# Kernel tuning notes

Hardware: AMD Instinct MI355X
Metric: run time of the kernel (lower is better)

## Reference

```python
import jax, jax.numpy as jnp
import numpy as np

G = 4      # num_groups
I = 128    # per-group input dim  (input_dim // num_groups)
H = 128    # per-group hidden dim (hidden_dim // num_groups)
B, T = 32, 1000


def setup_inputs() -> dict:
    key = jax.random.key(0)
    k0, k1, k2, k3, k4 = jax.random.split(key, 5)
    s = 1.0 / np.sqrt(H)  # PyTorch GRU init scale
    x = jax.random.normal(k0, (B, T, G * I), dtype=jnp.float32)
    w_ih = jax.random.uniform(k1, (G, 3 * H, I), jnp.float32, -s, s)
    w_hh = jax.random.uniform(k2, (G, 3 * H, H), jnp.float32, -s, s)
    b_ih = jax.random.uniform(k3, (G, 3 * H), jnp.float32, -s, s)
    b_hh = jax.random.uniform(k4, (G, 3 * H), jnp.float32, -s, s)
    return {"x": x, "w_ih": w_ih, "w_hh": w_hh, "b_ih": b_ih, "b_hh": b_hh}


def reference(x, w_ih, w_hh, b_ih, b_hh):
    # x: [B, T, G*I]. Chunking along dim 2 == reshape to [B, T, G, I].
    Bx, Tx, _ = x.shape
    xg = x.reshape(Bx, Tx, G, I)
    # Precompute input projections for all timesteps/groups (block-diagonal GEMM).
    gi = jnp.einsum('btgi,gki->btgk', xg, w_ih) + b_ih  # [B, T, G, 3H]

    def step(h, gi_t):
        # h: [B, G, H]; gi_t: [B, G, 3H]
        gh = jnp.einsum('bgh,gkh->bgk', h, w_hh) + b_hh  # [B, G, 3H]
        i_r, i_z, i_n = jnp.split(gi_t, 3, axis=-1)
        h_r, h_z, h_n = jnp.split(gh, 3, axis=-1)
        r = jax.nn.sigmoid(i_r + h_r)
        z = jax.nn.sigmoid(i_z + h_z)
        n = jnp.tanh(i_n + r * h_n)
        h_new = (1.0 - z) * n + z * h
        return h_new, h_new

    h0 = jnp.zeros((Bx, G, H), dtype=x.dtype)
    _, ys = jax.lax.scan(step, h0, jnp.swapaxes(gi, 0, 1))  # [T, B, G, H]
    # Concat of group outputs along dim 2 == reshape [B, T, G*H].
    return jnp.swapaxes(ys, 0, 1).reshape(Bx, Tx, G * H)
```

## Files before the change

### kernel.cpp

```cpp
#include <hip/hip_runtime.h>
#include <hip/hip_bf16.h>

#define NG 4
#define ID 128
#define HD 128
#define TH 384
#define NB 32
#define NT 1000
#define XW (NG*ID)
#define OW (NG*HD)

typedef _Float16 v8h __attribute__((ext_vector_type(8)));
typedef __attribute__((ext_vector_type(4))) float v4f;

__device__ __forceinline__ float sigm(float v) {
    return __fdividef(1.f, 1.f + __expf(-v));
}
__device__ __forceinline__ float tanh_(float v) {
    v = fminf(fmaxf(v, -15.f), 15.f);
    float e2 = __expf(2.f * v);
    return __fdividef(e2 - 1.f, e2 + 1.f);
}
__device__ __forceinline__ float sel4(v4f a, int s) {
    float x01 = (s & 1) ? a[1] : a[0];
    float x23 = (s & 1) ? a[3] : a[2];
    return (s & 2) ? x23 : x01;
}
__device__ __forceinline__ void gl2lds16(const void* g, void* l) {
    __builtin_amdgcn_global_load_lds(
        (const __attribute__((address_space(1))) unsigned int*)g,
        (__attribute__((address_space(3))) unsigned int*)l, 16, 0, 0);
}

__global__ __launch_bounds__(256) void gi_gemm4(
    const float* __restrict__ x,
    const float* __restrict__ w_ih,
    const float* __restrict__ b_ih,
    _Float16* __restrict__ gi_ws)
{
    const int tid = threadIdx.x;
    const int w   = tid >> 6, l = tid & 63;
    const int lr  = l & 15, lq = l >> 4;
    const int g   = blockIdx.z;
    const int b   = blockIdx.y >> 3;
    const int tt  = blockIdx.y & 7;
    const int gate = blockIdx.x;
    const int n0  = gate * 128 + (w >> 1) * 64;
    const int t0  = tt * 128 + (w & 1) * 64;

    v4f acc[4][4];
    #pragma unroll
    for (int mi = 0; mi < 4; ++mi)
        #pragma unroll
        for (int ni = 0; ni < 4; ++ni)
            acc[mi][ni] = (v4f){0.f, 0.f, 0.f, 0.f};

    #pragma unroll
    for (int kf = 0; kf < 4; ++kf) {
        v8h bf[4], af[4];
        #pragma unroll
        for (int ni = 0; ni < 4; ++ni) {
            const float* p = &w_ih[(size_t)(g * TH + n0 + ni * 16 + lr) * ID + kf * 32 + lq * 8];
            float4 f0 = *reinterpret_cast<const float4*>(p);
            float4 f1 = *reinterpret_cast<const float4*>(p + 4);
            v8h v;
            v[0]=(_Float16)f0.x; v[1]=(_Float16)f0.y; v[2]=(_Float16)f0.z; v[3]=(_Float16)f0.w;
            v[4]=(_Float16)f1.x; v[5]=(_Float16)f1.y; v[6]=(_Float16)f1.z; v[7]=(_Float16)f1.w;
            bf[ni] = v;
        }
        #pragma unroll
        for (int mi = 0; mi < 4; ++mi) {
            int trow = t0 + mi * 16 + lr;
            int tl = trow < NT ? trow : NT - 1;
            const float* p = &x[((size_t)b * NT + tl) * XW + g * ID + kf * 32 + lq * 8];
            float4 f0 = *reinterpret_cast<const float4*>(p);
            float4 f1 = *reinterpret_cast<const float4*>(p + 4);
            v8h v;
            v[0]=(_Float16)f0.x; v[1]=(_Float16)f0.y; v[2]=(_Float16)f0.z; v[3]=(_Float16)f0.w;
            v[4]=(_Float16)f1.x; v[5]=(_Float16)f1.y; v[6]=(_Float16)f1.z; v[7]=(_Float16)f1.w;
            af[mi] = v;
        }
        #pragma unroll
        for (int mi = 0; mi < 4; ++mi)
            #pragma unroll
            for (int ni = 0; ni < 4; ++ni)
                acc[mi][ni] = __builtin_amdgcn_mfma_f32_16x16x32_f16(
                    af[mi], bf[ni], acc[mi][ni], 0, 0, 0);
    }

    const size_t rbase = (size_t)(b * NG + g) * NT;
    #pragma unroll
    for (int ni = 0; ni < 4; ++ni) {
        const int col = n0 + ni * 16 + lr;
        const float bias = b_ih[g * TH + col];
        const int jj = col & 127;
        const int off = (gate == 0) ? jj * 2 : (gate == 1) ? jj * 2 + 1 : 256 + jj;
        #pragma unroll
        for (int mi = 0; mi < 4; ++mi) {
            #pragma unroll
            for (int r = 0; r < 4; ++r) {
                const int t = t0 + mi * 16 + lq * 4 + r;
                if (t < NT)
                    gi_ws[(rbase + t) * 384 + off] = (_Float16)(acc[mi][ni][r] + bias);
            }
        }
    }
}

__global__ __launch_bounds__(512) void gru_rec8(
    const _Float16* __restrict__ gi_ws,
    const float* __restrict__ w_hh,
    const float* __restrict__ b_hh,
    float* __restrict__ out)
{
    __shared__ __align__(16) _Float16 h_lds[2][128];
    __shared__ __align__(16) _Float16 tile[2][3072];

    const int tid = threadIdx.x;
    const int w = tid >> 6, l = tid & 63;
    const int lr = l & 15, lq = l >> 4;
    const int g = blockIdx.x & 3;
    const int b = blockIdx.x >> 2;

    v8h a[3][4];
    #pragma unroll
    for (int i = 0; i < 3; ++i) {
        const int mrow = i * 128 + 16 * w + lr;
        #pragma unroll
        for (int kf = 0; kf < 4; ++kf) {
            const float* p = &w_hh[(size_t)(g * TH + mrow) * HD + kf * 32 + lq * 8];
            float4 f0 = *reinterpret_cast<const float4*>(p);
            float4 f1 = *reinterpret_cast<const float4*>(p + 4);
            v8h v;
            v[0]=(_Float16)f0.x; v[1]=(_Float16)f0.y; v[2]=(_Float16)f0.z; v[3]=(_Float16)f0.w;
            v[4]=(_Float16)f1.x; v[5]=(_Float16)f1.y; v[6]=(_Float16)f1.z; v[7]=(_Float16)f1.w;
            a[i][kf] = v;
        }
    }

    const int sel = l & 3;
    const int j   = 16 * w + 4 * lq + sel;
    const bool active = ((l >> 2) & 3) == 0;
    const v4f bv0 = *reinterpret_cast<const v4f*>(&b_hh[g * TH +       16 * w + 4 * lq]);
    const v4f bv1 = *reinterpret_cast<const v4f*>(&b_hh[g * TH + 128 + 16 * w + 4 * lq]);
    const v4f bv2 = *reinterpret_cast<const v4f*>(&b_hh[g * TH + 256 + 16 * w + 4 * lq]);
    float hprev = 0.f;
    float* outp = out + (size_t)b * NT * OW + g * HD + j;

    if (tid < 128) { h_lds[0][tid] = (_Float16)0.f; h_lds[1][tid] = (_Float16)0.f; }

    const _Float16* gsrc = gi_ws + (size_t)(b * NG + g) * NT * 384;
    if (tid < 384) gl2lds16(gsrc + tid * 8, &tile[0][tid * 8]);
    __syncthreads();

    float hv[8];
    for (int T = 0; T < 125; ++T) {
        const int cbuf = T & 1;
        if (T < 124 && tid < 384)
            gl2lds16(gsrc + (size_t)(T + 1) * 3072 + tid * 8, &tile[cbuf ^ 1][tid * 8]);
        #pragma unroll
        for (int k = 0; k < 8; ++k) {
            const char* hb = reinterpret_cast<const char*>(&h_lds[k & 1][0]) + lq * 16;
            v8h f0 = *reinterpret_cast<const v8h*>(hb);
            v8h f1 = *reinterpret_cast<const v8h*>(hb + 64);
            v8h f2 = *reinterpret_cast<const v8h*>(hb + 128);
            v8h f3 = *reinterpret_cast<const v8h*>(hb + 192);
            v4f ac0 = bv0, ac1 = bv1, ac2 = bv2;
            ac0 = __builtin_amdgcn_mfma_f32_16x16x32_f16(a[0][0], f0, ac0, 0, 0, 0);
            ac1 = __builtin_amdgcn_mfma_f32_16x16x32_f16(a[1][0], f0, ac1, 0, 0, 0);
            ac2 = __builtin_amdgcn_mfma_f32_16x16x32_f16(a[2][0], f0, ac2, 0, 0, 0);
            ac0 = __builtin_amdgcn_mfma_f32_16x16x32_f16(a[0][1], f1, ac0, 0, 0, 0);
            ac1 = __builtin_amdgcn_mfma_f32_16x16x32_f16(a[1][1], f1, ac1, 0, 0, 0);
            ac2 = __builtin_amdgcn_mfma_f32_16x16x32_f16(a[2][1], f1, ac2, 0, 0, 0);
            ac0 = __builtin_amdgcn_mfma_f32_16x16x32_f16(a[0][2], f2, ac0, 0, 0, 0);
            ac1 = __builtin_amdgcn_mfma_f32_16x16x32_f16(a[1][2], f2, ac1, 0, 0, 0);
            ac2 = __builtin_amdgcn_mfma_f32_16x16x32_f16(a[2][2], f2, ac2, 0, 0, 0);
            ac0 = __builtin_amdgcn_mfma_f32_16x16x32_f16(a[0][3], f3, ac0, 0, 0, 0);
            ac1 = __builtin_amdgcn_mfma_f32_16x16x32_f16(a[1][3], f3, ac1, 0, 0, 0);
            ac2 = __builtin_amdgcn_mfma_f32_16x16x32_f16(a[2][3], f3, ac2, 0, 0, 0);

            float ghr = sel4(ac0, sel);
            float ghz = sel4(ac1, sel);
            float ghn = sel4(ac2, sel);

            const char* gl = reinterpret_cast<const char*>(&tile[cbuf][k * 384]);
            unsigned int rz = *reinterpret_cast<const unsigned int*>(gl + j * 4);
            float iN = (float)*reinterpret_cast<const _Float16*>(gl + 512 + j * 2);
            float iR = (float)__builtin_bit_cast(_Float16, (unsigned short)(rz & 0xffff));
            float iZ = (float)__builtin_bit_cast(_Float16, (unsigned short)(rz >> 16));

            float rr = sigm(iR + ghr);
            float zz = sigm(iZ + ghz);
            float nn = tanh_(fmaf(rr, ghn, iN));
            float hn = fmaf(zz, hprev - nn, nn);
            hprev = hn;
            hv[k] = hn;
            if (active) h_lds[(k + 1) & 1][j] = (_Float16)hn;
            __syncthreads();
        }
        if (active) {
            const size_t ob = (size_t)(T * 8) * OW;
            #pragma unroll
            for (int k = 0; k < 8; ++k)
                outp[ob + (size_t)k * OW] = hv[k];
        }
    }
}

extern "C" void kernel_launch(void* const* d_in, const int* in_sizes, int n_in,
                              void* d_out, int out_size, void* d_ws, size_t ws_size,
                              hipStream_t stream) {
    const float* x    = (const float*)d_in[0];
    const float* w_ih = (const float*)d_in[1];
    const float* w_hh = (const float*)d_in[2];
    const float* b_ih = (const float*)d_in[3];
    const float* b_hh = (const float*)d_in[4];
    float* out = (float*)d_out;
    _Float16* gi_ws = (_Float16*)d_ws;

    dim3 g1(3, NB * 8, NG);
    gi_gemm4<<<g1, 256, 0, stream>>>(x, w_ih, b_ih, gi_ws);
    gru_rec8<<<NB * NG, 512, 0, stream>>>(gi_ws, w_hh, b_hh, out);
}
```

Measured before the change: 581.4 us.

## Prefetch input gates into registers and replace syncthreads with LDS-only barrier

Removes the LDS double-buffered tile of precomputed input gates and instead has each thread load its own r/z/n values from global memory two timesteps ahead into registers. The per-step __syncthreads is replaced by an explicit lgkmcnt(0) wait plus s_barrier, so the barrier does not wait on outstanding global loads or stores. Output stores are issued per step rather than batched every 8 steps. This aims to shorten the serial per-step critical path, at the risk of global-load latency exceeding the two-step prefetch distance.

```diff
diff --git a/kernel.cpp b/kernel.cpp
--- a/kernel.cpp
+++ b/kernel.cpp
@@ -25,11 +25,6 @@
     float x01 = (s & 1) ? a[1] : a[0];
     float x23 = (s & 1) ? a[3] : a[2];
     return (s & 2) ? x23 : x01;
-}
-__device__ __forceinline__ void gl2lds16(const void* g, void* l) {
-    __builtin_amdgcn_global_load_lds(
-        (const __attribute__((address_space(1))) unsigned int*)g,
-        (__attribute__((address_space(3))) unsigned int*)l, 16, 0, 0);
 }
 
 __global__ __launch_bounds__(256) void gi_gemm4(
@@ -107,14 +102,13 @@
     }
 }
 
-__global__ __launch_bounds__(512) void gru_rec8(
+__global__ __launch_bounds__(512) void gru_rec9(
     const _Float16* __restrict__ gi_ws,
     const float* __restrict__ w_hh,
     const float* __restrict__ b_hh,
     float* __restrict__ out)
 {
     __shared__ __align__(16) _Float16 h_lds[2][128];
-    __shared__ __align__(16) _Float16 tile[2][3072];
 
     const int tid = threadIdx.x;
     const int w = tid >> 6, l = tid & 63;
@@ -150,61 +144,70 @@
     if (tid < 128) { h_lds[0][tid] = (_Float16)0.f; h_lds[1][tid] = (_Float16)0.f; }
 
     const _Float16* gsrc = gi_ws + (size_t)(b * NG + g) * NT * 384;
-    if (tid < 384) gl2lds16(gsrc + tid * 8, &tile[0][tid * 8]);
+
+    unsigned int rz0, rz1;
+    _Float16 nv0, nv1;
+    {
+        const _Float16* g0 = gsrc;
+        const _Float16* g1 = gsrc + 384;
+        rz0 = *reinterpret_cast<const unsigned int*>(g0 + j * 2);
+        nv0 = g0[256 + j];
+        rz1 = *reinterpret_cast<const unsigned int*>(g1 + j * 2);
+        nv1 = g1[256 + j];
+    }
     __syncthreads();
 
-    float hv[8];
-    for (int T = 0; T < 125; ++T) {
-        const int cbuf = T & 1;
-        if (T < 124 && tid < 384)
-            gl2lds16(gsrc + (size_t)(T + 1) * 3072 + tid * 8, &tile[cbuf ^ 1][tid * 8]);
-        #pragma unroll
-        for (int k = 0; k < 8; ++k) {
-            const char* hb = reinterpret_cast<const char*>(&h_lds[k & 1][0]) + lq * 16;
-            v8h f0 = *reinterpret_cast<const v8h*>(hb);
-            v8h f1 = *reinterpret_cast<const v8h*>(hb + 64);
-            v8h f2 = *reinterpret_cast<const v8h*>(hb + 128);
-            v8h f3 = *reinterpret_cast<const v8h*>(hb + 192);
-            v4f ac0 = bv0, ac1 = bv1, ac2 = bv2;
-            ac0 = __builtin_amdgcn_mfma_f32_16x16x32_f16(a[0][0], f0, ac0, 0, 0, 0);
-            ac1 = __builtin_amdgcn_mfma_f32_16x16x32_f16(a[1][0], f0, ac1, 0, 0, 0);
-            ac2 = __builtin_amdgcn_mfma_f32_16x16x32_f16(a[2][0], f0, ac2, 0, 0, 0);
-            ac0 = __builtin_amdgcn_mfma_f32_16x16x32_f16(a[0][1], f1, ac0, 0, 0, 0);
-            ac1 = __builtin_amdgcn_mfma_f32_16x16x32_f16(a[1][1], f1, ac1, 0, 0, 0);
-            ac2 = __builtin_amdgcn_mfma_f32_16x16x32_f16(a[2][1], f1, ac2, 0, 0, 0);
-            ac0 = __builtin_amdgcn_mfma_f32_16x16x32_f16(a[0][2], f2, ac0, 0, 0, 0);
-            ac1 = __builtin_amdgcn_mfma_f32_16x16x32_f16(a[1][2], f2, ac1, 0, 0, 0);
-            ac2 = __builtin_amdgcn_mfma_f32_16x16x32_f16(a[2][2], f2, ac2, 0, 0, 0);
-            ac0 = __builtin_amdgcn_mfma_f32_16x16x32_f16(a[0][3], f3, ac0, 0, 0, 0);
-            ac1 = __builtin_amdgcn_mfma_f32_16x16x32_f16(a[1][3], f3, ac1, 0, 0, 0);
-            ac2 = __builtin_amdgcn_mfma_f32_16x16x32_f16(a[2][3], f3, ac2, 0, 0, 0);
-
-            float ghr = sel4(ac0, sel);
-            float ghz = sel4(ac1, sel);
-            float ghn = sel4(ac2, sel);
-
-            const char* gl = reinterpret_cast<const char*>(&tile[cbuf][k * 384]);
-            unsigned int rz = *reinterpret_cast<const unsigned int*>(gl + j * 4);
-            float iN = (float)*reinterpret_cast<const _Float16*>(gl + 512 + j * 2);
-            float iR = (float)__builtin_bit_cast(_Float16, (unsigned short)(rz & 0xffff));
-            float iZ = (float)__builtin_bit_cast(_Float16, (unsigned short)(rz >> 16));
-
-            float rr = sigm(iR + ghr);
-            float zz = sigm(iZ + ghz);
-            float nn = tanh_(fmaf(rr, ghn, iN));
-            float hn = fmaf(zz, hprev - nn, nn);
-            hprev = hn;
-            hv[k] = hn;
-            if (active) h_lds[(k + 1) & 1][j] = (_Float16)hn;
-            __syncthreads();
-        }
-        if (active) {
-            const size_t ob = (size_t)(T * 8) * OW;
-            #pragma unroll
-            for (int k = 0; k < 8; ++k)
-                outp[ob + (size_t)k * OW] = hv[k];
-        }
-    }
+#define STEP(P, TCUR, RZ, NV)                                                      \
+    {                                                                              \
+        const char* hb = reinterpret_cast<const char*>(&h_lds[P][0]) + lq * 16;    \
+        v8h f0 = *reinterpret_cast<const v8h*>(hb);                                \
+        v8h f1 = *reinterpret_cast<const v8h*>(hb + 64);                           \
+        v8h f2 = *reinterpret_cast<const v8h*>(hb + 128);                          \
+        v8h f3 = *reinterpret_cast<const v8h*>(hb + 192);                          \
+        v4f ac0 = bv0, ac1 = bv1, ac2 = bv2;                                       \
+        ac0 = __builtin_amdgcn_mfma_f32_16x16x32_f16(a[0][0], f0, ac0, 0, 0, 0);   \
+        ac1 = __builtin_amdgcn_mfma_f32_16x16x32_f16(a[1][0], f0, ac1, 0, 0, 0);   \
+        ac2 = __builtin_amdgcn_mfma_f32_16x16x32_f16(a[2][0], f0, ac2, 0, 0, 0);   \
+        ac0 = __builtin_amdgcn_mfma_f32_16x16x32_f16(a[0][1], f1, ac0, 0, 0, 0);   \
+        ac1 = __builtin_amdgcn_mfma_f32_16x16x32_f16(a[1][1], f1, ac1, 0, 0, 0);   \
+        ac2 = __builtin_amdgcn_mfma_f32_16x16x32_f16(a[2][1], f1, ac2, 0, 0, 0);   \
+        ac0 = __builtin_amdgcn_mfma_f32_16x16x32_f16(a[0][2], f2, ac0, 0, 0, 0);   \
+        ac1 = __builtin_amdgcn_mfma_f32_16x16x32_f16(a[1][2], f2, ac1, 0, 0, 0);   \
+        ac2 = __builtin_amdgcn_mfma_f32_16x16x32_f16(a[2][2], f2, ac2, 0, 0, 0);   \
+        ac0 = __builtin_amdgcn_mfma_f32_16x16x32_f16(a[0][3], f3, ac0, 0, 0, 0);   \
+        ac1 = __builtin_amdgcn_mfma_f32_16x16x32_f16(a[1][3], f3, ac1, 0, 0, 0);   \
+        ac2 = __builtin_amdgcn_mfma_f32_16x16x32_f16(a[2][3], f3, ac2, 0, 0, 0);   \
+        float ghr = sel4(ac0, sel);                                                \
+        float ghz = sel4(ac1, sel);                                                \
+        float ghn = sel4(ac2, sel);                                                \
+        float iR = (float)__builtin_bit_cast(_Float16, (unsigned short)(RZ & 0xffff)); \
+        float iZ = (float)__builtin_bit_cast(_Float16, (unsigned short)(RZ >> 16));    \
+        float iN = (float)NV;                                                      \
+        float rr = sigm(iR + ghr);                                                 \
+        float zz = sigm(iZ + ghz);                                                 \
+        float nn = tanh_(fmaf(rr, ghn, iN));                                       \
+        float hn = fmaf(zz, hprev - nn, nn);                                       \
+        hprev = hn;                                                                \
+        if (active) {                                                              \
+            h_lds[(P) ^ 1][j] = (_Float16)hn;                                      \
+            outp[(size_t)(TCUR) * OW] = hn;                                        \
+        }                                                                          \
+        {                         \
+            int tl = (TCUR) + 2 < NT ? (TCUR) + 2 : NT - 1;                        \
+            const _Float16* gt = gsrc + (size_t)tl * 384;                          \
+            RZ = *reinterpret_cast<const unsigned int*>(gt + j * 2);               \
+            NV = gt[256 + j];                                                      \
+        }                                                                          \
+        asm volatile("s_waitcnt lgkmcnt(0)" ::: "memory");                         \
+        __builtin_amdgcn_s_barrier();                                              \
+        __builtin_amdgcn_sched_barrier(0);                                         \
+    }
+
+    for (int t = 0; t < NT; t += 2) {
+        STEP(0, t,     rz0, nv0)
+        STEP(1, t + 1, rz1, nv1)
+    }
+#undef STEP
 }
 
 extern "C" void kernel_launch(void* const* d_in, const int* in_sizes, int n_in,
@@ -220,5 +223,5 @@
 
     dim3 g1(3, NB * 8, NG);
     gi_gemm4<<<g1, 256, 0, stream>>>(x, w_ih, b_ih, gi_ws);
-    gru_rec8<<<NB * NG, 512, 0, stream>>>(gi_ws, w_hh, b_hh, out);
-}
+    gru_rec9<<<NB * NG, 512, 0, stream>>>(gi_ws, w_hh, b_hh, out);
+}
```

New measurement: 555.8 us. 4.4% less time.
